# Kernel optimization log

Hardware: AMD Instinct MI355X
Metric: run time of the kernel (lower is better)

Reference implementation:

```python
import jax, jax.numpy as jnp
import numpy as np

B, T, F, D, H, HD = 1, 16, 256, 768, 12, 64
NUM_LOOKBACK = 6  # remaining H - NUM_LOOKBACK heads are lookahead


def setup_inputs() -> dict:
    key = jax.random.key(0)
    ks = jax.random.split(key, 9)
    s = 0.02
    return {
        "x": jax.random.normal(ks[0], (B, T, F, D), dtype=jnp.float32),
        "Wq": jax.random.normal(ks[1], (H, D, HD), dtype=jnp.float32) * s,
        "bq": jax.random.normal(ks[2], (H, HD), dtype=jnp.float32) * s,
        "Wk": jax.random.normal(ks[3], (H, D, HD), dtype=jnp.float32) * s,
        "bk": jax.random.normal(ks[4], (H, HD), dtype=jnp.float32) * s,
        "Wv": jax.random.normal(ks[5], (H, D, HD), dtype=jnp.float32) * s,
        "bv": jax.random.normal(ks[6], (H, HD), dtype=jnp.float32) * s,
        "Wo": jax.random.normal(ks[7], (D, D), dtype=jnp.float32) * s,
        "bo": jax.random.normal(ks[8], (D,), dtype=jnp.float32) * s,
    }


def reference(x, Wq, bq, Wk, bk, Wv, bv, Wo, bo):
    b, t, f, d = x.shape
    tf = t * f
    xf = x.reshape(b, tf, d)

    # batched per-head projections: [b, h, n, hd]
    q = jnp.einsum('bnd,hdk->bhnk', xf, Wq) + bq[None, :, None, :]
    k = jnp.einsum('bnd,hdk->bhnk', xf, Wk) + bk[None, :, None, :]
    v = jnp.einsum('bnd,hdk->bhnk', xf, Wv) + bv[None, :, None, :]

    scale = 1.0 / jnp.sqrt(jnp.asarray(q.shape[-1], dtype=q.dtype))
    scores = jnp.einsum('bhqd,bhkd->bhqk', q, k) * scale  # [b,h,tf,tf]

    # lookback mask == causal (q_idx >= kv_idx); lookahead == anti-causal
    idx = jnp.arange(tf)
    causal = idx[:, None] >= idx[None, :]
    neg = jnp.finfo(scores.dtype).min
    s_lb = jnp.where(causal[None, None], scores[:, :NUM_LOOKBACK], neg)
    s_la = jnp.where(causal.T[None, None], scores[:, NUM_LOOKBACK:], neg)
    scores = jnp.concatenate([s_lb, s_la], axis=1)

    p = jax.nn.softmax(scores, axis=-1)
    o = jnp.einsum('bhqk,bhkd->bhqd', p, v)  # [b,h,tf,hd]
    o = o.transpose(0, 2, 1, 3).reshape(b, tf, d)  # concat heads on feature dim

    out = o @ Wo + bo
    return out.reshape(b, t, f, d)
```

## Files before the change

kernel.cpp:

```cpp
#include <hip/hip_runtime.h>
#include <hip/hip_bf16.h>

typedef __attribute__((ext_vector_type(4))) float f32x4;
typedef __attribute__((ext_vector_type(8))) short s16x8;
typedef __attribute__((ext_vector_type(4))) int i32x4;
typedef __attribute__((address_space(3))) unsigned char lds_t;
typedef __attribute__((address_space(1))) const unsigned char glob_t;

#define TFDIM 4096
#define DMODEL 768
#define NHEAD 12
#define HDIM 64
#define NLB 6

static __device__ __forceinline__ unsigned short f2bf(float f) {
    union { float f; unsigned u; } x; x.f = f;
    unsigned r = x.u + 0x7fff + ((x.u >> 16) & 1);
    return (unsigned short)(r >> 16);
}

static __device__ __forceinline__ float exp2_hw(float x) {
    float r;
    asm("v_exp_f32 %0, %1\n\ts_nop 0" : "=v"(r) : "v"(x));
    return r;
}

static __device__ __forceinline__ unsigned cvtpk_bf16(float lo, float hi) {
    unsigned r;
    asm("v_cvt_pk_bf16_f32 %0, %1, %2" : "=v"(r) : "v"(lo), "v"(hi));
    return r;
}

static __device__ __forceinline__ void xpose_pair(unsigned& a, unsigned& b) {
    asm volatile("v_permlane32_swap_b32 %0, %1" : "+v"(a), "+v"(b));
    asm volatile("v_permlane16_swap_b32 %0, %1" : "+v"(a), "+v"(b));
}

__global__ __launch_bounds__(256) void prep_kernel(
    const float* __restrict__ x, unsigned short* __restrict__ xb,
    const float* __restrict__ Wq, const float* __restrict__ Wk, const float* __restrict__ Wv,
    const float* __restrict__ bq, const float* __restrict__ bk, const float* __restrict__ bv,
    unsigned short* __restrict__ Wt, float* __restrict__ bias,
    const float* __restrict__ Wo, unsigned short* __restrict__ Wot,
    float* __restrict__ Lacc) {
    __shared__ unsigned short tile[64][65];
    int b = blockIdx.x;
    int t = threadIdx.x;
    if (b < 432) {
        int qkv = b / 144, rem = b - qkv * 144, h = rem / 12, kt = rem - h * 12;
        const float* W = (qkv == 0) ? Wq : ((qkv == 1) ? Wk : Wv);
        int trow = t >> 2, tco = (t & 3) << 4;
        const float* src = &W[((size_t)h * 768 + kt * 64 + trow) * 64 + tco];
#pragma unroll
        for (int j = 0; j < 4; j++) {
            float4 v = *(const float4*)&src[j * 4];
            tile[trow][tco + j * 4 + 0] = f2bf(v.x);
            tile[trow][tco + j * 4 + 1] = f2bf(v.y);
            tile[trow][tco + j * 4 + 2] = f2bf(v.z);
            tile[trow][tco + j * 4 + 3] = f2bf(v.w);
        }
        if (kt == 0 && t < 64) {
            const float* bb = (qkv == 0) ? bq : ((qkv == 1) ? bk : bv);
            bias[qkv * 768 + h * 64 + t] = bb[h * 64 + t];
        }
        __syncthreads();
        unsigned short vals[16];
#pragma unroll
        for (int j = 0; j < 16; j++) vals[j] = tile[tco + j][trow];
        unsigned short* dst = &Wt[(size_t)(qkv * 768 + h * 64 + trow) * 768 + kt * 64 + tco];
        *(s16x8*)&dst[0] = *(const s16x8*)&vals[0];
        *(s16x8*)&dst[8] = *(const s16x8*)&vals[8];
    } else if (b < 576) {
        int bb = b - 432;
        int nt = bb / 12, kt = bb - nt * 12;
        int trow = t >> 2, tco = (t & 3) << 4;
        const float* src = &Wo[(size_t)(kt * 64 + trow) * 768 + nt * 64 + tco];
#pragma unroll
        for (int j = 0; j < 4; j++) {
            float4 v = *(const float4*)&src[j * 4];
            tile[trow][tco + j * 4 + 0] = f2bf(v.x);
            tile[trow][tco + j * 4 + 1] = f2bf(v.y);
            tile[trow][tco + j * 4 + 2] = f2bf(v.z);
            tile[trow][tco + j * 4 + 3] = f2bf(v.w);
        }
        __syncthreads();
        unsigned short vals[16];
#pragma unroll
        for (int j = 0; j < 16; j++) vals[j] = tile[tco + j][trow];
        unsigned short* dst = &Wot[(size_t)(nt * 64 + trow) * 768 + kt * 64 + tco];
        *(s16x8*)&dst[0] = *(const s16x8*)&vals[0];
        *(s16x8*)&dst[8] = *(const s16x8*)&vals[8];
    } else if (b < 624) {
        int i = (b - 576) * 256 + t;
        if (i < NHEAD * TFDIM / 4) {
            float4 z = {0.f, 0.f, 0.f, 0.f};
            ((float4*)Lacc)[i] = z;
        }
    } else {
        int i = (b - 624) * 256 + t;
        if (i < TFDIM * DMODEL / 4) {
            float4 v = ((const float4*)x)[i];
            ushort4 o;
            o.x = f2bf(v.x); o.y = f2bf(v.y); o.z = f2bf(v.z); o.w = f2bf(v.w);
            ((ushort4*)xb)[i] = o;
        }
    }
}


template <int EPI, int ANORM>
__global__ __launch_bounds__(256) void gemm_bt_kernel(
    const unsigned short* __restrict__ A,
    const float* __restrict__ Af32, const float* __restrict__ Lacc,
    const unsigned short* __restrict__ Bt,
    const float* __restrict__ bias,
    float* __restrict__ Cf, unsigned short* __restrict__ Cb,
    unsigned short* __restrict__ Vtg,
    int M, int N, int K) {
    __shared__ __align__(16) unsigned short As[128 * 64];
    __shared__ __align__(16) unsigned short Bs[128 * 64];
    int tid = threadIdx.x;
    int w = tid >> 6, l = tid & 63, lr = l & 15, lg = l >> 4;
    int wm = w >> 1, wn = w & 1;

    int nwg = gridDim.x * gridDim.y;
    int flat = blockIdx.y * gridDim.x + blockIdx.x;
    int cpx = nwg >> 3;
    int swz = (flat & 7) * cpx + (flat >> 3);
    int bx = swz % gridDim.x, by = swz / gridDim.x;
    size_t mbase = (size_t)by * 128, nbase = (size_t)bx * 128;

    int drw = l >> 3, dslot = l & 7;
    int dg = (dslot ^ drw) << 3;
    f32x4 acc[4][4] = {};
    for (int k0 = 0; k0 < K; k0 += 64) {
        __syncthreads();
        if (ANORM) {
#pragma unroll
            for (int i = 0; i < 4; i++) {
                int idx = tid + i * 256;
                int row = idx >> 3, g = idx & 7;
                const float* src = &Af32[(mbase + row) * K + k0 + g * 8];
                float4 a0 = *(const float4*)&src[0];
                float4 a1 = *(const float4*)&src[4];
                float rl = __builtin_amdgcn_rcpf(Lacc[(size_t)(k0 >> 6) * TFDIM + mbase + row]);
                unsigned short us[8];
                us[0] = f2bf(a0.x * rl); us[1] = f2bf(a0.y * rl);
                us[2] = f2bf(a0.z * rl); us[3] = f2bf(a0.w * rl);
                us[4] = f2bf(a1.x * rl); us[5] = f2bf(a1.y * rl);
                us[6] = f2bf(a1.z * rl); us[7] = f2bf(a1.w * rl);
                *(s16x8*)&As[row * 64 + ((g ^ (row & 7)) << 3)] = *(const s16x8*)us;
            }
        } else {
#pragma unroll
            for (int j = 0; j < 4; j++) {
                int row = j * 32 + w * 8 + drw;
                __builtin_amdgcn_global_load_lds((glob_t*)&A[(mbase + row) * K + k0 + dg],
                                                 (lds_t*)&As[(j * 32 + w * 8) * 64], 16, 0, 0);
            }
        }
#pragma unroll
        for (int j = 0; j < 4; j++) {
            int row = j * 32 + w * 8 + drw;
            __builtin_amdgcn_global_load_lds((glob_t*)&Bt[(nbase + row) * K + k0 + dg],
                                             (lds_t*)&Bs[(j * 32 + w * 8) * 64], 16, 0, 0);
        }
        __syncthreads();
#pragma unroll
        for (int ks = 0; ks < 2; ks++) {
            s16x8 af[4], bfr[4];
#pragma unroll
            for (int m = 0; m < 4; m++) {
                int row = wm * 64 + m * 16 + lr;
                af[m] = *(const s16x8*)&As[row * 64 + (((ks * 4 + lg) ^ (row & 7)) << 3)];
            }
#pragma unroll
            for (int n = 0; n < 4; n++) {
                int row = wn * 64 + n * 16 + lr;
                bfr[n] = *(const s16x8*)&Bs[row * 64 + (((ks * 4 + lg) ^ (row & 7)) << 3)];
            }
#pragma unroll
            for (int m = 0; m < 4; m++)
#pragma unroll
                for (int n = 0; n < 4; n++)
                    acc[m][n] = __builtin_amdgcn_mfma_f32_16x16x32_bf16(af[m], bfr[n], acc[m][n], 0, 0, 0);
        }
    }
#pragma unroll
    for (int m = 0; m < 4; m++) {
        size_t row0 = mbase + wm * 64 + m * 16 + lg * 4;
#pragma unroll
        for (int n = 0; n < 4; n++) {
            size_t col = nbase + wn * 64 + n * 16 + lr;
            float bv = bias[col];
#pragma unroll
            for (int r = 0; r < 4; r++) {
                float v = acc[m][n][r] + bv;
                if (EPI == 0) {
                    Cf[(row0 + r) * N + col] = v;
                } else if (col < 1536) {
                    if (col < 768) v *= 0.18033688f;
                    Cb[(((col >> 6) * 4096 + (row0 + r)) << 6) + (col & 63)] = f2bf(v);
                } else {
                    Vtg[(size_t)(((col - 1536) >> 6) * 262144) + (col & 63) * 4096 + (row0 + r)] = f2bf(v);
                }
            }
        }
    }
}

__global__ __launch_bounds__(512, 4) void attn_kernel(const unsigned short* __restrict__ qk,
                                                      const unsigned short* __restrict__ vtg,
                                                      float* __restrict__ Oacc,
                                                      float* __restrict__ Lacc) {
    __shared__ __align__(16) unsigned short Ks[3][64][64];
    __shared__ __align__(16) unsigned short Vs[3][64][64];

    int b = blockIdx.x;
    int h = b % NHEAD;
    int idx = 79 - (b / NHEAD);
    int jqw, c, n;
    if (idx < 8)       { jqw = idx;               c = 0;              n = 1; }
    else if (idx < 24) { jqw = 8 + ((idx - 8) >> 1);  c = (idx - 8) & 1;  n = 2; }
    else if (idx < 48) { jqw = 16 + (idx - 24) / 3;   c = (idx - 24) % 3; n = 3; }
    else               { jqw = 24 + ((idx - 48) >> 2); c = (idx - 48) & 3; n = 4; }
    int W = 2 * jqw + 2;
    int base = W / n, rem = W % n;
    int len = base + (c < rem ? 1 : 0);
    int s0 = c * base + (c < rem ? c : rem);
    bool causal = (h < NLB);
    int jq = causal ? jqw : (31 - jqw);
    int qbase = jq * 128;
    int dkb = 2 * jq;
    int kb0 = (causal ? 0 : (62 - 2 * jqw)) + s0;
    int kb1 = kb0 + len - 1;

    const unsigned short* Q  = qk + (size_t)h * TFDIM * HDIM;
    const unsigned short* Kp = qk + (size_t)(NHEAD + h) * TFDIM * HDIM;
    const unsigned short* Vt = vtg + (size_t)h * HDIM * TFDIM;

    int tid = threadIdx.x, w = tid >> 6, l = tid & 63, lr = l & 15, lg = l >> 4;
    int qh = w >> 2, wq = w & 3;
    int dk = dkb + qh;

    s16x8 qf[2];
    {
        size_t qrow = (size_t)(qbase + qh * 64 + wq * 16 + lr);
        qf[0] = *(const s16x8*)&Q[qrow * HDIM + lg * 8];
        qf[1] = *(const s16x8*)&Q[qrow * HDIM + 32 + lg * 8];
    }
    f32x4 oacc[4] = {};
    float lsum = 0.f;

    int drow = tid >> 3, dseg = tid & 7;
    int sg0 = (dseg ^ (drow & 7)) << 3;
    auto stage = [&](int buf, int kv) {
        __builtin_amdgcn_global_load_lds((glob_t*)(Kp + (size_t)(kv * 64 + drow) * HDIM + sg0),
                                         (lds_t*)&Ks[buf][w * 8][0], 16, 0, 0);
        __builtin_amdgcn_global_load_lds((glob_t*)(Vt + (size_t)drow * TFDIM + kv * 64 + sg0),
                                         (lds_t*)&Vs[buf][w * 8][0], 16, 0, 0);
    };

    stage(0, kb0);

    int cur = 0;
    int qcol = wq * 16 + lr;
    for (int kb = kb0; kb <= kb1; kb++) {
        bool more = (kb < kb1);
        if (more) {
            int nxt = (cur == 2) ? 0 : cur + 1;
            stage(nxt, kb + 1);
            asm volatile("s_waitcnt vmcnt(2)" ::: "memory");
        } else {
            asm volatile("s_waitcnt vmcnt(0)" ::: "memory");
        }
        __builtin_amdgcn_s_barrier();
        __builtin_amdgcn_sched_barrier(0);

        int kvbase = kb * 64;
        s16x8 vf[2][4];
#pragma unroll
        for (int ks = 0; ks < 2; ks++)
#pragma unroll
            for (int df = 0; df < 4; df++)
                vf[ks][df] = *(const s16x8*)&Vs[cur][df * 16 + lr][(ks * 32 + lg * 8) ^ ((lr & 7) << 3)];
        f32x4 s[4];
        __builtin_amdgcn_s_setprio(1);
#pragma unroll
        for (int f = 0; f < 4; f++) {
            s16x8 kf0 = *(const s16x8*)&Ks[cur][f * 16 + lr][(lg * 8) ^ ((lr & 7) << 3)];
            s16x8 kf1 = *(const s16x8*)&Ks[cur][f * 16 + lr][(32 + lg * 8) ^ ((lr & 7) << 3)];
            f32x4 z = {0.f, 0.f, 0.f, 0.f};
            z = __builtin_amdgcn_mfma_f32_16x16x32_bf16(kf0, qf[0], z, 0, 0, 0);
            z = __builtin_amdgcn_mfma_f32_16x16x32_bf16(kf1, qf[1], z, 0, 0, 0);
            s[f] = z;
        }
        __builtin_amdgcn_s_setprio(0);

        bool skip = causal ? (kb > dk) : (kb < dk);
        if (!skip) {
            if (kb == dk) {
                int qi = qbase + qh * 64 + qcol;
#pragma unroll
                for (int f = 0; f < 4; f++)
#pragma unroll
                    for (int r = 0; r < 4; r++) {
                        int ki = kvbase + f * 16 + lg * 4 + r;
                        bool keep = causal ? (qi >= ki) : (qi <= ki);
                        if (!keep) s[f][r] = -1e30f;
                    }
            }
            float ls = 0.f;
            unsigned w0[4], w1[4];
#pragma unroll
            for (int f = 0; f < 4; f++) {
                float p0 = exp2_hw(s[f][0]);
                float p1 = exp2_hw(s[f][1]);
                float p2 = exp2_hw(s[f][2]);
                float p3 = exp2_hw(s[f][3]);
                ls += (p0 + p1) + (p2 + p3);
                w0[f] = cvtpk_bf16(p0, p1);
                w1[f] = cvtpk_bf16(p2, p3);
            }
            lsum += ls;
            xpose_pair(w0[0], w0[1]);
            xpose_pair(w1[0], w1[1]);
            xpose_pair(w0[2], w0[3]);
            xpose_pair(w1[2], w1[3]);
            union { unsigned u[4]; s16x8 v8; } pk0, pk1;
            pk0.u[0] = w0[0]; pk0.u[1] = w1[0]; pk0.u[2] = w0[1]; pk0.u[3] = w1[1];
            pk1.u[0] = w0[2]; pk1.u[1] = w1[2]; pk1.u[2] = w0[3]; pk1.u[3] = w1[3];
            __builtin_amdgcn_s_setprio(1);
#pragma unroll
            for (int df = 0; df < 4; df++) {
                oacc[df] = __builtin_amdgcn_mfma_f32_16x16x32_bf16(pk0.v8, vf[0][df], oacc[df], 0, 0, 0);
                oacc[df] = __builtin_amdgcn_mfma_f32_16x16x32_bf16(pk1.v8, vf[1][df], oacc[df], 0, 0, 0);
            }
            __builtin_amdgcn_s_setprio(0);
        }

        cur = (cur == 2) ? 0 : cur + 1;
    }
    lsum += __shfl_xor(lsum, 16);
    lsum += __shfl_xor(lsum, 32);
    if (lg == 0)
        atomicAdd(&Lacc[h * TFDIM + qbase + qh * 64 + wq * 16 + lr], lsum);
#pragma unroll
    for (int df = 0; df < 4; df++)
#pragma unroll
        for (int r = 0; r < 4; r++) {
            int row = qbase + qh * 64 + wq * 16 + lg * 4 + r;
            atomicAdd(&Oacc[(size_t)row * DMODEL + h * HDIM + df * 16 + lr], oacc[df][r]);
        }
}

__global__ void merge_kernel(const float* __restrict__ Oacc, const float* __restrict__ Lacc,
                             unsigned short* __restrict__ ob) {
    int i = blockIdx.x * 256 + threadIdx.x;
    if (i >= TFDIM * DMODEL / 4) return;
    int col4 = i % (DMODEL / 4), row = i / (DMODEL / 4);
    float4 v = ((const float4*)Oacc)[i];
    int h = col4 >> 4;
    float rl = 1.0f / Lacc[h * TFDIM + row];
    ushort4 u;
    u.x = f2bf(v.x * rl); u.y = f2bf(v.y * rl); u.z = f2bf(v.z * rl); u.w = f2bf(v.w * rl);
    ((ushort4*)ob)[i] = u;
}


extern "C" void kernel_launch(void* const* d_in, const int* in_sizes, int n_in,
                              void* d_out, int out_size, void* d_ws, size_t ws_size,
                              hipStream_t stream) {
    const float* x  = (const float*)d_in[0];
    const float* Wq = (const float*)d_in[1];
    const float* bq = (const float*)d_in[2];
    const float* Wk = (const float*)d_in[3];
    const float* bk = (const float*)d_in[4];
    const float* Wv = (const float*)d_in[5];
    const float* bv = (const float*)d_in[6];
    const float* Wo = (const float*)d_in[7];
    const float* bo = (const float*)d_in[8];
    float* out = (float*)d_out;
    char* ws = (char*)d_ws;
    const unsigned short* dummyA = (const unsigned short*)d_ws;

    if (ws_size >= 32833536) {
        float*          Oacc = (float*)(ws + 0);
        unsigned short* xb   = (unsigned short*)(ws + 0);
        unsigned short* WtQ  = (unsigned short*)(ws + 6291456);
        float*          bqkv = (float*)(ws + 9830400);
        unsigned short* qkb  = (unsigned short*)(ws + 12582912);
        unsigned short* vtg  = (unsigned short*)(ws + 25165824);
        unsigned short* Wot  = (unsigned short*)(ws + 31457280);
        float*          Lacc = (float*)(ws + 32636928);

        prep_kernel<<<3696, 256, 0, stream>>>(x, xb, Wq, Wk, Wv, bq, bk, bv, WtQ, bqkv, Wo, Wot, Lacc);

        dim3 g1(2304 / 128, 4096 / 128);
        gemm_bt_kernel<1, 0><<<g1, 256, 0, stream>>>(xb, nullptr, nullptr, WtQ, bqkv, nullptr, qkb, vtg, 4096, 2304, 768);

        hipMemsetAsync(Oacc, 0, (size_t)TFDIM * DMODEL * 4, stream);

        attn_kernel<<<960, 512, 0, stream>>>(qkb, vtg, Oacc, Lacc);

        dim3 g3(768 / 128, 4096 / 128);
        gemm_bt_kernel<0, 1><<<g3, 256, 0, stream>>>(dummyA, Oacc, Lacc, Wot, bo, out, nullptr, nullptr, 4096, 768, 768);
    } else {
        unsigned short* xb   = (unsigned short*)(ws + 0);
        unsigned short* ob   = (unsigned short*)(ws + 0);
        unsigned short* WtQ  = (unsigned short*)(ws + 6291456);
        unsigned short* Wot  = (unsigned short*)(ws + 9830400);
        float*          bqkv = (float*)(ws + 11010048);
        unsigned short* qkb  = (unsigned short*)(ws + 11019264);
        unsigned short* vtg  = (unsigned short*)(ws + 23602176);
        float*          Lacc = (float*)(ws + 29893632);
        float*          Oacc = out;

        hipMemsetAsync(Oacc, 0, (size_t)TFDIM * DMODEL * 4, stream);
        prep_kernel<<<3696, 256, 0, stream>>>(x, xb, Wq, Wk, Wv, bq, bk, bv, WtQ, bqkv, Wo, Wot, Lacc);

        dim3 g1(2304 / 128, 4096 / 128);
        gemm_bt_kernel<1, 0><<<g1, 256, 0, stream>>>(xb, nullptr, nullptr, WtQ, bqkv, nullptr, qkb, vtg, 4096, 2304, 768);

        attn_kernel<<<960, 512, 0, stream>>>(qkb, vtg, Oacc, Lacc);
        merge_kernel<<<(TFDIM * DMODEL / 4 + 255) / 256, 256, 0, stream>>>(Oacc, Lacc, ob);

        dim3 g3(768 / 128, 4096 / 128);
        gemm_bt_kernel<0, 0><<<g3, 256, 0, stream>>>(ob, nullptr, nullptr, Wot, bo, out, nullptr, nullptr, 4096, 768, 768);
    }
}
```

Baseline: 128.2 us.

## Double attention Q tile to 256 rows per block to reuse K/V tiles

Each attention block now processes 256 query rows: every wave holds two 16-row Q fragments (A and B), 128 rows apart, and reuses each staged K/V LDS tile for both. The work split across blocks is rebuilt with a triangular chunking scheme (72 work items per head, 864 blocks). The aim is to halve K/V global loads and LDS staging per query row and cut the number of partial-output atomics. In exchange, per-thread register use roughly doubles, which may reduce occupancy at launch bounds (512,4), and V fragments are now read from LDS inside the PV loop.

Result: slower. 144.8 us (+13.0%).

```diff
diff --git a/kernel.cpp b/kernel.cpp
--- a/kernel.cpp
+++ b/kernel.cpp
@@ -107,7 +107,6 @@
     }
 }
 
-
 template <int EPI, int ANORM>
 __global__ __launch_bounds__(256) void gemm_bt_kernel(
     const unsigned short* __restrict__ A,
@@ -218,21 +217,23 @@
 
     int b = blockIdx.x;
     int h = b % NHEAD;
-    int idx = 79 - (b / NHEAD);
-    int jqw, c, n;
-    if (idx < 8)       { jqw = idx;               c = 0;              n = 1; }
-    else if (idx < 24) { jqw = 8 + ((idx - 8) >> 1);  c = (idx - 8) & 1;  n = 2; }
-    else if (idx < 48) { jqw = 16 + (idx - 24) / 3;   c = (idx - 24) % 3; n = 3; }
-    else               { jqw = 24 + ((idx - 48) >> 2); c = (idx - 48) & 3; n = 4; }
-    int W = 2 * jqw + 2;
-    int base = W / n, rem = W % n;
-    int len = base + (c < rem ? 1 : 0);
-    int s0 = c * base + (c < rem ? c : rem);
+    int c = 71 - (b / NHEAD);
+    int m = 0;
+    while ((m + 1) * (m + 2) <= c) m++;
+    int d = c - m * (m + 1);
+    int nch = m + 1;
+    int half = (d >= nch) ? 1 : 0;
+    int jqw = 2 * m + half;
+    int sub = d - half * nch;
+    int W = 4 * jqw + 4;
+    int base = W / nch, rem = W % nch;
+    int len = base + (sub < rem ? 1 : 0);
+    int s0 = sub * base + (sub < rem ? sub : rem);
     bool causal = (h < NLB);
-    int jq = causal ? jqw : (31 - jqw);
-    int qbase = jq * 128;
-    int dkb = 2 * jq;
-    int kb0 = (causal ? 0 : (62 - 2 * jqw)) + s0;
+    int jq = causal ? jqw : (15 - jqw);
+    int qbase = jq * 256;
+    int dkb = 4 * jq;
+    int kb0 = (causal ? 0 : (60 - 4 * jqw)) + s0;
     int kb1 = kb0 + len - 1;
 
     const unsigned short* Q  = qk + (size_t)h * TFDIM * HDIM;
@@ -240,17 +241,20 @@
     const unsigned short* Vt = vtg + (size_t)h * HDIM * TFDIM;
 
     int tid = threadIdx.x, w = tid >> 6, l = tid & 63, lr = l & 15, lg = l >> 4;
-    int qh = w >> 2, wq = w & 3;
-    int dk = dkb + qh;
-
-    s16x8 qf[2];
+    int dkA = dkb + (w >> 2);
+    int dkB = dkb + 2 + (w >> 2);
+
+    s16x8 qfA[2], qfB[2];
     {
-        size_t qrow = (size_t)(qbase + qh * 64 + wq * 16 + lr);
-        qf[0] = *(const s16x8*)&Q[qrow * HDIM + lg * 8];
-        qf[1] = *(const s16x8*)&Q[qrow * HDIM + 32 + lg * 8];
-    }
-    f32x4 oacc[4] = {};
-    float lsum = 0.f;
+        size_t qrA = (size_t)(qbase + w * 16 + lr);
+        qfA[0] = *(const s16x8*)&Q[qrA * HDIM + lg * 8];
+        qfA[1] = *(const s16x8*)&Q[qrA * HDIM + 32 + lg * 8];
+        size_t qrB = qrA + 128;
+        qfB[0] = *(const s16x8*)&Q[qrB * HDIM + lg * 8];
+        qfB[1] = *(const s16x8*)&Q[qrB * HDIM + 32 + lg * 8];
+    }
+    f32x4 oaccA[4] = {}, oaccB[4] = {};
+    float lsumA = 0.f, lsumB = 0.f;
 
     int drow = tid >> 3, dseg = tid & 7;
     int sg0 = (dseg ^ (drow & 7)) << 3;
@@ -264,7 +268,6 @@
     stage(0, kb0);
 
     int cur = 0;
-    int qcol = wq * 16 + lr;
     for (int kb = kb0; kb <= kb1; kb++) {
         bool more = (kb < kb1);
         if (more) {
@@ -278,29 +281,31 @@
         __builtin_amdgcn_sched_barrier(0);
 
         int kvbase = kb * 64;
-        s16x8 vf[2][4];
-#pragma unroll
-        for (int ks = 0; ks < 2; ks++)
-#pragma unroll
-            for (int df = 0; df < 4; df++)
-                vf[ks][df] = *(const s16x8*)&Vs[cur][df * 16 + lr][(ks * 32 + lg * 8) ^ ((lr & 7) << 3)];
-        f32x4 s[4];
+        f32x4 sA[4], sB[4];
         __builtin_amdgcn_s_setprio(1);
 #pragma unroll
         for (int f = 0; f < 4; f++) {
             s16x8 kf0 = *(const s16x8*)&Ks[cur][f * 16 + lr][(lg * 8) ^ ((lr & 7) << 3)];
             s16x8 kf1 = *(const s16x8*)&Ks[cur][f * 16 + lr][(32 + lg * 8) ^ ((lr & 7) << 3)];
-            f32x4 z = {0.f, 0.f, 0.f, 0.f};
-            z = __builtin_amdgcn_mfma_f32_16x16x32_bf16(kf0, qf[0], z, 0, 0, 0);
-            z = __builtin_amdgcn_mfma_f32_16x16x32_bf16(kf1, qf[1], z, 0, 0, 0);
-            s[f] = z;
+            f32x4 zA = {0.f, 0.f, 0.f, 0.f};
+            zA = __builtin_amdgcn_mfma_f32_16x16x32_bf16(kf0, qfA[0], zA, 0, 0, 0);
+            zA = __builtin_amdgcn_mfma_f32_16x16x32_bf16(kf1, qfA[1], zA, 0, 0, 0);
+            sA[f] = zA;
+            f32x4 zB = {0.f, 0.f, 0.f, 0.f};
+            zB = __builtin_amdgcn_mfma_f32_16x16x32_bf16(kf0, qfB[0], zB, 0, 0, 0);
+            zB = __builtin_amdgcn_mfma_f32_16x16x32_bf16(kf1, qfB[1], zB, 0, 0, 0);
+            sB[f] = zB;
         }
         __builtin_amdgcn_s_setprio(0);
 
-        bool skip = causal ? (kb > dk) : (kb < dk);
-        if (!skip) {
+        bool doA = causal ? (kb <= dkA) : (kb >= dkA);
+        bool doB = causal ? (kb <= dkB) : (kb >= dkB);
+
+        union { unsigned u[4]; s16x8 v8; } pkA0, pkA1, pkB0, pkB1;
+        auto softmax_pack = [&](int dk, int qrow0, f32x4 (&s)[4], float& lsum,
+                                unsigned* u0, unsigned* u1) {
             if (kb == dk) {
-                int qi = qbase + qh * 64 + qcol;
+                int qi = qrow0 + lr;
 #pragma unroll
                 for (int f = 0; f < 4; f++)
 #pragma unroll
@@ -327,30 +332,48 @@
             xpose_pair(w1[0], w1[1]);
             xpose_pair(w0[2], w0[3]);
             xpose_pair(w1[2], w1[3]);
-            union { unsigned u[4]; s16x8 v8; } pk0, pk1;
-            pk0.u[0] = w0[0]; pk0.u[1] = w1[0]; pk0.u[2] = w0[1]; pk0.u[3] = w1[1];
-            pk1.u[0] = w0[2]; pk1.u[1] = w1[2]; pk1.u[2] = w0[3]; pk1.u[3] = w1[3];
+            u0[0] = w0[0]; u0[1] = w1[0]; u0[2] = w0[1]; u0[3] = w1[1];
+            u1[0] = w0[2]; u1[1] = w1[2]; u1[2] = w0[3]; u1[3] = w1[3];
+        };
+        if (doA) softmax_pack(dkA, qbase + w * 16, sA, lsumA, pkA0.u, pkA1.u);
+        if (doB) softmax_pack(dkB, qbase + 128 + w * 16, sB, lsumB, pkB0.u, pkB1.u);
+
+        if (doA || doB) {
             __builtin_amdgcn_s_setprio(1);
 #pragma unroll
             for (int df = 0; df < 4; df++) {
-                oacc[df] = __builtin_amdgcn_mfma_f32_16x16x32_bf16(pk0.v8, vf[0][df], oacc[df], 0, 0, 0);
-                oacc[df] = __builtin_amdgcn_mfma_f32_16x16x32_bf16(pk1.v8, vf[1][df], oacc[df], 0, 0, 0);
+                s16x8 vf0 = *(const s16x8*)&Vs[cur][df * 16 + lr][(lg * 8) ^ ((lr & 7) << 3)];
+                s16x8 vf1 = *(const s16x8*)&Vs[cur][df * 16 + lr][(32 + lg * 8) ^ ((lr & 7) << 3)];
+                if (doA) {
+                    oaccA[df] = __builtin_amdgcn_mfma_f32_16x16x32_bf16(pkA0.v8, vf0, oaccA[df], 0, 0, 0);
+                    oaccA[df] = __builtin_amdgcn_mfma_f32_16x16x32_bf16(pkA1.v8, vf1, oaccA[df], 0, 0, 0);
+                }
+                if (doB) {
+                    oaccB[df] = __builtin_amdgcn_mfma_f32_16x16x32_bf16(pkB0.v8, vf0, oaccB[df], 0, 0, 0);
+                    oaccB[df] = __builtin_amdgcn_mfma_f32_16x16x32_bf16(pkB1.v8, vf1, oaccB[df], 0, 0, 0);
+                }
             }
             __builtin_amdgcn_s_setprio(0);
         }
 
         cur = (cur == 2) ? 0 : cur + 1;
     }
-    lsum += __shfl_xor(lsum, 16);
-    lsum += __shfl_xor(lsum, 32);
-    if (lg == 0)
-        atomicAdd(&Lacc[h * TFDIM + qbase + qh * 64 + wq * 16 + lr], lsum);
+    lsumA += __shfl_xor(lsumA, 16);
+    lsumA += __shfl_xor(lsumA, 32);
+    lsumB += __shfl_xor(lsumB, 16);
+    lsumB += __shfl_xor(lsumB, 32);
+    if (lg == 0) {
+        atomicAdd(&Lacc[h * TFDIM + qbase + w * 16 + lr], lsumA);
+        atomicAdd(&Lacc[h * TFDIM + qbase + 128 + w * 16 + lr], lsumB);
+    }
 #pragma unroll
     for (int df = 0; df < 4; df++)
 #pragma unroll
         for (int r = 0; r < 4; r++) {
-            int row = qbase + qh * 64 + wq * 16 + lg * 4 + r;
-            atomicAdd(&Oacc[(size_t)row * DMODEL + h * HDIM + df * 16 + lr], oacc[df][r]);
+            int rowA = qbase + w * 16 + lg * 4 + r;
+            atomicAdd(&Oacc[(size_t)rowA * DMODEL + h * HDIM + df * 16 + lr], oaccA[df][r]);
+            int rowB = rowA + 128;
+            atomicAdd(&Oacc[(size_t)rowB * DMODEL + h * HDIM + df * 16 + lr], oaccB[df][r]);
         }
 }
 
@@ -401,7 +424,7 @@
 
         hipMemsetAsync(Oacc, 0, (size_t)TFDIM * DMODEL * 4, stream);
 
-        attn_kernel<<<960, 512, 0, stream>>>(qkb, vtg, Oacc, Lacc);
+        attn_kernel<<<864, 512, 0, stream>>>(qkb, vtg, Oacc, Lacc);
 
         dim3 g3(768 / 128, 4096 / 128);
         gemm_bt_kernel<0, 1><<<g3, 256, 0, stream>>>(dummyA, Oacc, Lacc, Wot, bo, out, nullptr, nullptr, 4096, 768, 768);
@@ -422,7 +445,7 @@
         dim3 g1(2304 / 128, 4096 / 128);
         gemm_bt_kernel<1, 0><<<g1, 256, 0, stream>>>(xb, nullptr, nullptr, WtQ, bqkv, nullptr, qkb, vtg, 4096, 2304, 768);
 
-        attn_kernel<<<960, 512, 0, stream>>>(qkb, vtg, Oacc, Lacc);
+        attn_kernel<<<864, 512, 0, stream>>>(qkb, vtg, Oacc, Lacc);
         merge_kernel<<<(TFDIM * DMODEL / 4 + 255) / 256, 256, 0, stream>>>(Oacc, Lacc, ob);
 
         dim3 g3(768 / 128, 4096 / 128);
```
